# Kernel optimization log

Measured on AMD Instinct MI355X. Metric: run time of the kernel, lower is better.

The kernel has to match this reference:

```python
import jax, jax.numpy as jnp
import numpy as np

B, S, D_MODEL, H = 2, 2048, 1024, 16
DIMS = D_MODEL // H  # 64


def setup_inputs() -> dict:
    key = jax.random.key(0)
    ks = jax.random.split(key, 7)
    scale = 1.0 / np.sqrt(D_MODEL)
    x = jax.random.normal(ks[0], (B, S, D_MODEL), dtype=jnp.float32)
    # Stacked per-head projection params: nn.Linear(d_model, dims) per head
    Wq = jax.random.uniform(ks[1], (H, DIMS, D_MODEL), minval=-scale, maxval=scale, dtype=jnp.float32)
    Wk = jax.random.uniform(ks[2], (H, DIMS, D_MODEL), minval=-scale, maxval=scale, dtype=jnp.float32)
    Wv = jax.random.uniform(ks[3], (H, DIMS, D_MODEL), minval=-scale, maxval=scale, dtype=jnp.float32)
    bq = jax.random.uniform(ks[4], (H, DIMS), minval=-scale, maxval=scale, dtype=jnp.float32)
    bk = jax.random.uniform(ks[5], (H, DIMS), minval=-scale, maxval=scale, dtype=jnp.float32)
    bv = jax.random.uniform(ks[6], (H, DIMS), minval=-scale, maxval=scale, dtype=jnp.float32)
    return {"x": x, "Wq": Wq, "Wk": Wk, "Wv": Wv, "bq": bq, "bk": bk, "bv": bv}


def reference(x, Wq, Wk, Wv, bq, bk, bv):
    # Per-head linear projections: [B,S,D] x [H,E,D] -> [B,H,S,E]
    q = jnp.einsum('bsd,hed->bhse', x, Wq) + bq[None, :, None, :]
    k = jnp.einsum('bsd,hed->bhse', x, Wk) + bk[None, :, None, :]
    v = jnp.einsum('bsd,hed->bhse', x, Wv) + bv[None, :, None, :]
    norm = DIMS ** (-0.5)
    # (q @ k^T) * norm @ v  -- NO softmax, as in the source
    scores = jnp.einsum('bhse,bhte->bhst', q, k) * norm  # [B,H,S,S]
    out = jnp.einsum('bhst,bhte->bhse', scores, v)       # [B,H,S,E]
    # concat heads along feature dim (head order matches torch.cat)
    return out.transpose(0, 2, 1, 3).reshape(B, S, H * DIMS)
```

## Files before the change

### kernel.cpp

```cpp
#include <hip/hip_runtime.h>


typedef __attribute__((ext_vector_type(8))) __bf16 bf16x8;
typedef __attribute__((ext_vector_type(8))) short short8;
typedef __attribute__((ext_vector_type(4))) float f32x4;
typedef __attribute__((ext_vector_type(4))) unsigned short ushort4v;

#define NX  4194304
#define NW1 1048576
#define NW  3145728

__device__ __forceinline__ float bf2f(unsigned short u) {
  union { unsigned int i; float f; } v; v.i = ((unsigned int)u) << 16; return v.f;
}
__device__ __forceinline__ unsigned short f2bf(float f) {
  union { float f; unsigned int i; } v; v.f = f;
  unsigned int u = v.i;
  u += 0x7fffu + ((u >> 16) & 1u);
  return (unsigned short)(u >> 16);
}

__device__ __forceinline__ void gload_lds16(const void* g, void* l) {
  __builtin_amdgcn_global_load_lds(
      (const __attribute__((address_space(1))) void*)(unsigned long long)(g),
      (__attribute__((address_space(3))) void*)(unsigned int)(unsigned long long)(l),
      16, 0, 0);
}

__global__ __launch_bounds__(256) void convert_pack(
    const float* __restrict__ x,
    const float* __restrict__ wq, const float* __restrict__ wk,
    const float* __restrict__ wv,
    const float* __restrict__ bq, const float* __restrict__ bk,
    const float* __restrict__ bv,
    unsigned short* __restrict__ Xbf, unsigned short* __restrict__ Wcat,
    float* __restrict__ Bcat)
{
  const long long t8 = ((long long)blockIdx.x * 256 + threadIdx.x) * 8;
  const float* src;
  unsigned short* dst;
  long long off;
  if (t8 < NX) {
    src = x; dst = Xbf; off = t8;
  } else if (t8 < NX + NW) {
    const long long w = t8 - NX;
    const int z = (int)(w >> 20);
    off = w & (NW1 - 1);
    src = (z == 0) ? wq : (z == 1) ? wk : wv;
    dst = Wcat + (long long)z * NW1;
  } else if (t8 < NX + NW + 3072) {
    const long long bo = t8 - (NX + NW);
    const int z = (int)(bo >> 10);
    const long long o2 = bo & 1023;
    const float* bsrc = (z == 0) ? bq : (z == 1) ? bk : bv;
    *(f32x4*)(Bcat + z * 1024 + o2)     = *(const f32x4*)(bsrc + o2);
    *(f32x4*)(Bcat + z * 1024 + o2 + 4) = *(const f32x4*)(bsrc + o2 + 4);
    return;
  } else {
    return;
  }
  f32x4 v0 = *(const f32x4*)(src + off);
  f32x4 v1 = *(const f32x4*)(src + off + 4);
  union { short8 s; unsigned short u[8]; } o;
#pragma unroll
  for (int j = 0; j < 4; ++j) {
    o.u[j]     = f2bf(v0[j]);
    o.u[4 + j] = f2bf(v1[j]);
  }
  *(short8*)(dst + off) = o.s;
}

__global__ __launch_bounds__(256, 2) void qkv_gemm(
    const unsigned short* __restrict__ Xbf,
    const unsigned short* __restrict__ Wcat,
    const float* __restrict__ Bcat,
    unsigned short* __restrict__ Qt,
    unsigned short* __restrict__ Kt,
    unsigned short* __restrict__ Vt)
{
  __shared__ unsigned short smA[128 * 64];
  __shared__ unsigned short smB[128 * 64];

  const int tid = threadIdx.x;
  int bid = blockIdx.x;
  bid = (bid & 7) * 96 + (bid >> 3);
  const int colBase = (bid % 24) * 128;
  const int rowBase = (bid / 24) * 128;

  const int lane = tid & 63;
  const int wid  = tid >> 6;
  const int wr = (wid >> 1) * 64;
  const int wc = (wid & 1) * 64;
  const int lr = lane & 15;
  const int lk = lane >> 4;

  f32x4 acc[4][4] = {};

  for (int kt = 0; kt < 16; ++kt) {
    const int k0 = kt * 64;
#pragma unroll
    for (int i = 0; i < 4; ++i) {
      const int si = i * 256 + tid;
      const int row = si >> 3, seg = si & 7;
      const int sseg = seg ^ (row & 7);
      gload_lds16(Xbf  + (size_t)(rowBase + row) * 1024 + k0 + sseg * 8,
                  smA + (si & ~63) * 8);
      gload_lds16(Wcat + (size_t)(colBase + row) * 1024 + k0 + sseg * 8,
                  smB + (si & ~63) * 8);
    }
    __syncthreads();

#pragma unroll
    for (int ks = 0; ks < 2; ++ks) {
      bf16x8 av[4], bv4[4];
#pragma unroll
      for (int m = 0; m < 4; ++m) {
        const int row = wr + m * 16 + lr;
        av[m] = *(const bf16x8*)((const char*)smA + row * 128 +
                                 (((ks * 4 + lk) ^ (row & 7)) * 16));
      }
#pragma unroll
      for (int n = 0; n < 4; ++n) {
        const int row = wc + n * 16 + lr;
        bv4[n] = *(const bf16x8*)((const char*)smB + row * 128 +
                                  (((ks * 4 + lk) ^ (row & 7)) * 16));
      }
#pragma unroll
      for (int m = 0; m < 4; ++m)
#pragma unroll
        for (int n = 0; n < 4; ++n)
          acc[m][n] = __builtin_amdgcn_mfma_f32_16x16x32_bf16(av[m], bv4[n], acc[m][n], 0, 0, 0);
    }
    __syncthreads();
  }

  const int zone = colBase >> 10;
  unsigned short* __restrict__ T = (zone == 0) ? Qt : (zone == 1) ? Kt : Vt;
  const int bB = rowBase >> 11;
#pragma unroll
  for (int n = 0; n < 4; ++n) {
    const int colG = colBase + wc + n * 16 + lr;
    const float bval = Bcat[colG];
    const int hf = (colG >> 6) & 15;
    const int f  = colG & 63;
    const size_t rowOff = ((size_t)(bB * 16 + hf) * 64 + f) * 2048;
#pragma unroll
    for (int m = 0; m < 4; ++m) {
      const int t = (rowBase + wr + m * 16 + lk * 4) & 2047;
      ushort4v pk;
#pragma unroll
      for (int j = 0; j < 4; ++j)
        pk[j] = f2bf(acc[m][n][j] + bval);
      *(ushort4v*)&T[rowOff + t] = pk;
    }
  }
}

__global__ __launch_bounds__(64) void kv_outer(
    const unsigned short* __restrict__ Kt,
    const unsigned short* __restrict__ Vt,
    float* __restrict__ Mpart)
{
  const int lane = threadIdx.x;
  const int blk = blockIdx.x;
  const int bh = blk >> 3, tc = blk & 7;
  const int lr = lane & 15, lk = lane >> 4;
  const size_t base = (size_t)bh * 64 * 2048;

  f32x4 acc[4][4] = {};
#pragma unroll
  for (int ks = 0; ks < 8; ++ks) {
    const int t0 = tc * 256 + ks * 32 + lk * 8;
    bf16x8 af[4], bf[4];
#pragma unroll
    for (int m = 0; m < 4; ++m)
      af[m] = *(const bf16x8*)&Kt[base + (size_t)(m * 16 + lr) * 2048 + t0];
#pragma unroll
    for (int n = 0; n < 4; ++n)
      bf[n] = *(const bf16x8*)&Vt[base + (size_t)(n * 16 + lr) * 2048 + t0];
#pragma unroll
    for (int m = 0; m < 4; ++m)
#pragma unroll
      for (int n = 0; n < 4; ++n)
        acc[m][n] = __builtin_amdgcn_mfma_f32_16x16x32_bf16(af[m], bf[n], acc[m][n], 0, 0, 0);
  }
  float* out = Mpart + (size_t)blk * 4096;
#pragma unroll
  for (int m = 0; m < 4; ++m)
#pragma unroll
    for (int n = 0; n < 4; ++n)
#pragma unroll
      for (int j = 0; j < 4; ++j)
        out[(m * 16 + lk * 4 + j) * 64 + n * 16 + lr] = acc[m][n][j];
}

__global__ __launch_bounds__(256) void m_reduce(
    const float* __restrict__ Mpart, float* __restrict__ M)
{
  const int bh = blockIdx.x;
  const int tid = threadIdx.x;
#pragma unroll
  for (int i = 0; i < 4; ++i) {
    const int off = i * 1024 + tid * 4;
    f32x4 s = {};
#pragma unroll
    for (int ch = 0; ch < 8; ++ch)
      s += *(const f32x4*)&Mpart[((size_t)bh * 8 + ch) * 4096 + off];
    s *= 0.125f;
    *(f32x4*)&M[(size_t)bh * 4096 + off] = s;
  }
}

__global__ __launch_bounds__(256) void qm_out(
    const unsigned short* __restrict__ Qt, const float* __restrict__ M,
    float* __restrict__ Out)
{
  __shared__ float Ms[64 * 64];
  __shared__ float Qst[64 * 132];
  const int tid = threadIdx.x;
  const int b = blockIdx.z, h = blockIdx.y, s0 = blockIdx.x * 128;
  const int bh = b * 16 + h;

#pragma unroll
  for (int i = 0; i < 4; ++i) {
    const int off = i * 1024 + tid * 4;
    *(f32x4*)&Ms[off] = *(const f32x4*)&M[(size_t)bh * 4096 + off];
  }
  const size_t qbase = (size_t)bh * 64 * 2048;
#pragma unroll
  for (int i = 0; i < 4; ++i) {
    const int slot = i * 256 + tid;
    const int f = slot >> 4, c = slot & 15;
    short8 q = *(const short8*)&Qt[qbase + (size_t)f * 2048 + s0 + c * 8];
#pragma unroll
    for (int j = 0; j < 8; ++j)
      Qst[f * 132 + c * 8 + j] = bf2f((unsigned short)q[j]);
  }
  __syncthreads();

  const int s = (tid >> 3) * 4;
  const int e0 = (tid & 7) * 8;
  float acc2[4][8] = {};
  for (int f = 0; f < 64; ++f) {
    f32x4 m0 = *(const f32x4*)&Ms[f * 64 + e0];
    f32x4 m1 = *(const f32x4*)&Ms[f * 64 + e0 + 4];
#pragma unroll
    for (int i = 0; i < 4; ++i) {
      const float q = Qst[f * 132 + s + i];
#pragma unroll
      for (int j = 0; j < 4; ++j) {
        acc2[i][j]     += q * m0[j];
        acc2[i][j + 4] += q * m1[j];
      }
    }
  }
  const size_t obase = ((size_t)b * 2048 + s0) * 1024 + h * 64;
#pragma unroll
  for (int i = 0; i < 4; ++i) {
    f32x4 o0 = { acc2[i][0], acc2[i][1], acc2[i][2], acc2[i][3] };
    f32x4 o1 = { acc2[i][4], acc2[i][5], acc2[i][6], acc2[i][7] };
    *(f32x4*)&Out[obase + (size_t)(s + i) * 1024 + e0]     = o0;
    *(f32x4*)&Out[obase + (size_t)(s + i) * 1024 + e0 + 4] = o1;
  }
}

extern "C" void kernel_launch(void* const* d_in, const int* in_sizes, int n_in,
                              void* d_out, int out_size, void* d_ws, size_t ws_size,
                              hipStream_t stream) {
  const float* x  = (const float*)d_in[0];
  const float* Wq = (const float*)d_in[1];
  const float* Wk = (const float*)d_in[2];
  const float* Wv = (const float*)d_in[3];
  const float* bq = (const float*)d_in[4];
  const float* bk = (const float*)d_in[5];
  const float* bv = (const float*)d_in[6];
  float* out = (float*)d_out;

  char* ws = (char*)d_ws;
  const size_t MiB = 1024ull * 1024ull;
  unsigned short* Xbf   = (unsigned short*)(ws);
  unsigned short* Wcat  = (unsigned short*)(ws + 8  * MiB);
  float*          Bcat  = (float*)         (ws + 14 * MiB);
  unsigned short* Qt    = (unsigned short*)(ws + 15 * MiB);
  unsigned short* Kt    = (unsigned short*)(ws + 23 * MiB);
  unsigned short* Vt    = (unsigned short*)(ws + 31 * MiB);
  float*          Mpart = (float*)         (ws + 39 * MiB);
  float*          Mfin  = (float*)         (ws + 43 * MiB);

  convert_pack<<<3586, 256, 0, stream>>>(x, Wq, Wk, Wv, bq, bk, bv,
                                         Xbf, Wcat, Bcat);
  qkv_gemm<<<768, 256, 0, stream>>>(Xbf, Wcat, Bcat, Qt, Kt, Vt);
  kv_outer<<<256, 64, 0, stream>>>(Kt, Vt, Mpart);
  m_reduce<<<32, 256, 0, stream>>>(Mpart, Mfin);
  qm_out<<<dim3(16, 16, 2), 256, 0, stream>>>(Qt, Mfin, out);
}
```

Before: 65.36 us.

## Retile QKV GEMM to 256x192 double-buffered blocks and fold M reduction into qm_out

The QKV projection GEMM moves from 128x128 tiles with 256 threads to 256x192 tiles with 512 threads. It double-buffers LDS with async global-to-LDS loads, prefetching two K-steps ahead, and uses explicit vmcnt waits and barriers in place of __syncthreads. The grid drops from 768 to 256 blocks, one per CU, and each block reuses its tiles more. The separate m_reduce launch is removed, and each qm_out block now sums the 8 partial K^T V chunks itself. This saves a launch but repeats the reduction in all 16 blocks per head. The larger tile uses 112KB of LDS and a big accumulator set, which limits occupancy.

```diff
diff --git a/kernel.cpp b/kernel.cpp
--- a/kernel.cpp
+++ b/kernel.cpp
@@ -70,7 +70,10 @@
   *(short8*)(dst + off) = o.s;
 }
 
-__global__ __launch_bounds__(256, 2) void qkv_gemm(
+#define ABYTES 32768
+#define BBYTES 24576
+#define BUFB   57344
+__global__ __launch_bounds__(512, 2) void qkv_gemm(
     const unsigned short* __restrict__ Xbf,
     const unsigned short* __restrict__ Wcat,
     const float* __restrict__ Bcat,
@@ -78,74 +81,106 @@
     unsigned short* __restrict__ Kt,
     unsigned short* __restrict__ Vt)
 {
-  __shared__ unsigned short smA[128 * 64];
-  __shared__ unsigned short smB[128 * 64];
+  __shared__ unsigned char lds[2 * BUFB];
 
   const int tid = threadIdx.x;
   int bid = blockIdx.x;
-  bid = (bid & 7) * 96 + (bid >> 3);
-  const int colBase = (bid % 24) * 128;
-  const int rowBase = (bid / 24) * 128;
+  bid = (bid & 7) * 32 + (bid >> 3);
+  const int colBase = (bid & 15) * 192;
+  const int rowBase = (bid >> 4) * 256;
 
   const int lane = tid & 63;
   const int wid  = tid >> 6;
-  const int wr = (wid >> 1) * 64;
-  const int wc = (wid & 1) * 64;
+  const int wm = wid >> 2;
+  const int wn = wid & 3;
+  const int wr = wm * 128;
+  const int wc = wn * 48;
   const int lr = lane & 15;
   const int lk = lane >> 4;
 
-  f32x4 acc[4][4] = {};
-
-  for (int kt = 0; kt < 16; ++kt) {
-    const int k0 = kt * 64;
-#pragma unroll
-    for (int i = 0; i < 4; ++i) {
-      const int si = i * 256 + tid;
-      const int row = si >> 3, seg = si & 7;
-      const int sseg = seg ^ (row & 7);
-      gload_lds16(Xbf  + (size_t)(rowBase + row) * 1024 + k0 + sseg * 8,
-                  smA + (si & ~63) * 8);
-      gload_lds16(Wcat + (size_t)(colBase + row) * 1024 + k0 + sseg * 8,
-                  smB + (si & ~63) * 8);
+  const int sArow[4] = { (0*512+tid) >> 3, (1*512+tid) >> 3,
+                         (2*512+tid) >> 3, (3*512+tid) >> 3 };
+  const int sseg = tid & 7;
+
+  f32x4 acc[8][3] = {};
+
+#define STAGE(buf, kt)                                                        \
+  {                                                                           \
+    const int k0_ = (kt) * 64;                                                \
+    _Pragma("unroll")                                                         \
+    for (int i_ = 0; i_ < 4; ++i_) {                                          \
+      const int row_ = sArow[i_];                                             \
+      const int ss_ = sseg ^ (row_ & 7);                                      \
+      gload_lds16(Xbf + (size_t)(rowBase + row_) * 1024 + k0_ + ss_ * 8,      \
+                  lds + (buf) * BUFB + (i_ * 512 + tid) * 16);                \
+    }                                                                         \
+    _Pragma("unroll")                                                         \
+    for (int i_ = 0; i_ < 3; ++i_) {                                          \
+      const int row_ = sArow[i_];                                             \
+      const int ss_ = sseg ^ (row_ & 7);                                      \
+      gload_lds16(Wcat + (size_t)(colBase + row_) * 1024 + k0_ + ss_ * 8,     \
+                  lds + (buf) * BUFB + ABYTES + (i_ * 512 + tid) * 16);       \
+    }                                                                         \
+  }
+
+  STAGE(0, 0);
+  STAGE(1, 1);
+  asm volatile("s_waitcnt vmcnt(7)" ::: "memory");
+  __builtin_amdgcn_s_barrier();
+
+  for (int t = 0; t < 16; ++t) {
+    const int cur = t & 1;
+    const unsigned char* Ab = lds + cur * BUFB;
+    const unsigned char* Bb = Ab + ABYTES;
+
+    bf16x8 af[2][8], bvf[2][3];
+#pragma unroll
+    for (int ks = 0; ks < 2; ++ks) {
+#pragma unroll
+      for (int m = 0; m < 8; ++m) {
+        const int row = wr + m * 16 + lr;
+        af[ks][m] = *(const bf16x8*)(Ab + row * 128 +
+                                     (((ks * 4 + lk) ^ (row & 7)) * 16));
+      }
+#pragma unroll
+      for (int n = 0; n < 3; ++n) {
+        const int row = wc + n * 16 + lr;
+        bvf[ks][n] = *(const bf16x8*)(Bb + row * 128 +
+                                      (((ks * 4 + lk) ^ (row & 7)) * 16));
+      }
     }
-    __syncthreads();
-
-#pragma unroll
-    for (int ks = 0; ks < 2; ++ks) {
-      bf16x8 av[4], bv4[4];
-#pragma unroll
-      for (int m = 0; m < 4; ++m) {
-        const int row = wr + m * 16 + lr;
-        av[m] = *(const bf16x8*)((const char*)smA + row * 128 +
-                                 (((ks * 4 + lk) ^ (row & 7)) * 16));
-      }
-#pragma unroll
-      for (int n = 0; n < 4; ++n) {
-        const int row = wc + n * 16 + lr;
-        bv4[n] = *(const bf16x8*)((const char*)smB + row * 128 +
-                                  (((ks * 4 + lk) ^ (row & 7)) * 16));
-      }
-#pragma unroll
-      for (int m = 0; m < 4; ++m)
-#pragma unroll
-        for (int n = 0; n < 4; ++n)
-          acc[m][n] = __builtin_amdgcn_mfma_f32_16x16x32_bf16(av[m], bv4[n], acc[m][n], 0, 0, 0);
-    }
-    __syncthreads();
-  }
-
-  const int zone = colBase >> 10;
-  unsigned short* __restrict__ T = (zone == 0) ? Qt : (zone == 1) ? Kt : Vt;
+    asm volatile("s_waitcnt lgkmcnt(0)" ::: "memory");
+    __builtin_amdgcn_s_barrier();
+
+    if (t + 2 < 16) STAGE(cur, t + 2);
+
+#pragma unroll
+    for (int ks = 0; ks < 2; ++ks)
+#pragma unroll
+      for (int m = 0; m < 8; ++m)
+#pragma unroll
+        for (int n = 0; n < 3; ++n)
+          acc[m][n] = __builtin_amdgcn_mfma_f32_16x16x32_bf16(
+              af[ks][m], bvf[ks][n], acc[m][n], 0, 0, 0);
+
+    if (t < 13) asm volatile("s_waitcnt vmcnt(7)" ::: "memory");
+    else        asm volatile("s_waitcnt vmcnt(0)" ::: "memory");
+    __builtin_amdgcn_s_barrier();
+  }
+#undef STAGE
+
   const int bB = rowBase >> 11;
 #pragma unroll
-  for (int n = 0; n < 4; ++n) {
+  for (int n = 0; n < 3; ++n) {
     const int colG = colBase + wc + n * 16 + lr;
     const float bval = Bcat[colG];
+    const int zone = colG >> 10;
+    unsigned short* __restrict__ T = (zone == 0) ? Qt : (zone == 1) ? Kt : Vt;
     const int hf = (colG >> 6) & 15;
     const int f  = colG & 63;
     const size_t rowOff = ((size_t)(bB * 16 + hf) * 64 + f) * 2048;
 #pragma unroll
-    for (int m = 0; m < 4; ++m) {
+    for (int m = 0; m < 8; ++m) {
       const int t = (rowBase + wr + m * 16 + lk * 4) & 2047;
       ushort4v pk;
 #pragma unroll
@@ -194,25 +229,8 @@
         out[(m * 16 + lk * 4 + j) * 64 + n * 16 + lr] = acc[m][n][j];
 }
 
-__global__ __launch_bounds__(256) void m_reduce(
-    const float* __restrict__ Mpart, float* __restrict__ M)
-{
-  const int bh = blockIdx.x;
-  const int tid = threadIdx.x;
-#pragma unroll
-  for (int i = 0; i < 4; ++i) {
-    const int off = i * 1024 + tid * 4;
-    f32x4 s = {};
-#pragma unroll
-    for (int ch = 0; ch < 8; ++ch)
-      s += *(const f32x4*)&Mpart[((size_t)bh * 8 + ch) * 4096 + off];
-    s *= 0.125f;
-    *(f32x4*)&M[(size_t)bh * 4096 + off] = s;
-  }
-}
-
 __global__ __launch_bounds__(256) void qm_out(
-    const unsigned short* __restrict__ Qt, const float* __restrict__ M,
+    const unsigned short* __restrict__ Qt, const float* __restrict__ Mpart,
     float* __restrict__ Out)
 {
   __shared__ float Ms[64 * 64];
@@ -224,7 +242,12 @@
 #pragma unroll
   for (int i = 0; i < 4; ++i) {
     const int off = i * 1024 + tid * 4;
-    *(f32x4*)&Ms[off] = *(const f32x4*)&M[(size_t)bh * 4096 + off];
+    f32x4 s = {};
+#pragma unroll
+    for (int ch = 0; ch < 8; ++ch)
+      s += *(const f32x4*)&Mpart[((size_t)bh * 8 + ch) * 4096 + off];
+    s *= 0.125f;
+    *(f32x4*)&Ms[off] = s;
   }
   const size_t qbase = (size_t)bh * 64 * 2048;
 #pragma unroll
@@ -285,12 +308,10 @@
   unsigned short* Kt    = (unsigned short*)(ws + 23 * MiB);
   unsigned short* Vt    = (unsigned short*)(ws + 31 * MiB);
   float*          Mpart = (float*)         (ws + 39 * MiB);
-  float*          Mfin  = (float*)         (ws + 43 * MiB);
 
   convert_pack<<<3586, 256, 0, stream>>>(x, Wq, Wk, Wv, bq, bk, bv,
                                          Xbf, Wcat, Bcat);
-  qkv_gemm<<<768, 256, 0, stream>>>(Xbf, Wcat, Bcat, Qt, Kt, Vt);
+  qkv_gemm<<<256, 512, 0, stream>>>(Xbf, Wcat, Bcat, Qt, Kt, Vt);
   kv_outer<<<256, 64, 0, stream>>>(Kt, Vt, Mpart);
-  m_reduce<<<32, 256, 0, stream>>>(Mpart, Mfin);
-  qm_out<<<dim3(16, 16, 2), 256, 0, stream>>>(Qt, Mfin, out);
-}
+  qm_out<<<dim3(16, 16, 2), 256, 0, stream>>>(Qt, Mpart, out);
+}
```

Result: slower. 66.95 us (+2.4%).
